# Optimization experiments

Hardware: AMD Instinct MI355X
Metric: run time of the kernel (lower is better)

Reference implementation:

```python
import jax, jax.numpy as jnp
import numpy as np

MARGIN = 0.3
ANCHOR = 0.5
EPS = 1e-8  # torch F.cosine_similarity default eps


def _cosine(a, b):
    # a: [N, D], b: [D] -> [N]
    num = a @ b
    den = jnp.maximum(jnp.linalg.norm(a, axis=-1) * jnp.linalg.norm(b), EPS)
    return num / den


def setup_inputs() -> dict:
    key = jax.random.key(0)
    k1, k2, k3, k4 = jax.random.split(key, 4)
    N, D = 8192, 1024
    return {
        "q_emb": jax.random.normal(k1, (D,), dtype=jnp.float32),
        "d_embs": jax.random.normal(k2, (N, D), dtype=jnp.float32),
        "c_emb": jax.random.normal(k3, (D,), dtype=jnp.float32),
        "rates": jax.random.uniform(k4, (N,), dtype=jnp.float32),
    }


def reference(q_emb, d_embs, c_emb, rates):
    # cosine similarity of each distractor vs question / correct answer
    s_q = _cosine(d_embs, q_emb)          # [N]
    _s_c = _cosine(d_embs, c_emb)         # [N] computed in original, never used
    quality = jnp.abs(rates - ANCHOR)     # [N]

    # Vectorized form of the nested i,j loop:
    # pair (i, j) contributes relu(margin + s_q[j] - s_q[i]) iff quality[i] > quality[j]
    mask = quality[:, None] > quality[None, :]              # [N, N]; diagonal is False
    pair_loss = jax.nn.relu(MARGIN + s_q[None, :] - s_q[:, None])  # [N, N]
    total = jnp.sum(jnp.where(mask, pair_loss, jnp.float32(0.0)))
    n_pairs = jnp.sum(mask)
    return total / jnp.maximum(n_pairs, 1).astype(total.dtype)
```

## Files before the change

### kernel.cpp

```cpp
#include <hip/hip_runtime.h>

#define MARGIN 0.3f
#define ANCHOR 0.5f
#define EPS    1e-8f
#define BI     1024
#define BJ     64
#define NSLOT  32

typedef unsigned long long ull;


__global__ __launch_bounds__(256) void sq_kernel(
        const float* __restrict__ q, const float* __restrict__ d,
        const float* __restrict__ rates, float2* __restrict__ pairs,
        char* __restrict__ acc, int N, int D) {
    int tid = threadIdx.x;
    if (blockIdx.x == 0) {
        if (tid < NSLOT)          *(double*)  (acc + (size_t)tid * 64)               = 0.0;
        else if (tid < 2 * NSLOT) *(unsigned*)(acc + 2048 + (size_t)(tid - 32) * 64) = 0u;
    }
    int wave = (blockIdx.x * blockDim.x + tid) >> 6;
    int lane = tid & 63;
    if (wave >= N) return;
    const float* row = d + (size_t)wave * (size_t)D;

    float dot = 0.f, dn = 0.f, qn = 0.f;
    for (int it = lane * 4; it < D; it += 256) {
        float4 dv = *(const float4*)(row + it);
        float4 qv = *(const float4*)(q + it);
        dot += dv.x * qv.x + dv.y * qv.y + dv.z * qv.z + dv.w * qv.w;
        dn  += dv.x * dv.x + dv.y * dv.y + dv.z * dv.z + dv.w * dv.w;
        qn  += qv.x * qv.x + qv.y * qv.y + qv.z * qv.z + qv.w * qv.w;
    }
    #pragma unroll
    for (int off = 32; off >= 1; off >>= 1) {
        dot += __shfl_xor(dot, off);
        dn  += __shfl_xor(dn,  off);
        qn  += __shfl_xor(qn,  off);
    }
    if (lane == 0) {
        float den = fmaxf(sqrtf(dn) * sqrtf(qn), EPS);
        pairs[wave] = make_float2(dot / den, fabsf(rates[wave] - ANCHOR));
    }
}

__global__ __launch_bounds__(256) void pair_kernel(
        const float2* __restrict__ pairs,
        int N, char* __restrict__ acc) {
    __shared__ float2   tile[BJ];
    __shared__ double   bsum[4];
    __shared__ unsigned bcnt[4];

    int tid = threadIdx.x;
    int ib  = blockIdx.x * BI;
    int j0  = blockIdx.y * BJ;

    if (tid < BJ) {
        int j = j0 + tid;
        tile[tid] = (j < N) ? pairs[j] : make_float2(0.f, 1e30f);
    }
    __syncthreads();

    float a0 = 0.f, g0 = -1.f, a1 = 0.f, g1 = -1.f;
    float a2 = 0.f, g2 = -1.f, a3 = 0.f, g3 = -1.f;
    {
        int i;
        float2 p;
        i = ib + tid;        if (i < N) { p = pairs[i]; a0 = MARGIN - p.x; g0 = p.y; }
        i = ib + tid + 256;  if (i < N) { p = pairs[i]; a1 = MARGIN - p.x; g1 = p.y; }
        i = ib + tid + 512;  if (i < N) { p = pairs[i]; a2 = MARGIN - p.x; g2 = p.y; }
        i = ib + tid + 768;  if (i < N) { p = pairs[i]; a3 = MARGIN - p.x; g3 = p.y; }
    }

    float    s0 = 0.f, s1 = 0.f, s2 = 0.f, s3 = 0.f;
    unsigned c  = 0;
    #pragma unroll 8
    for (int j = 0; j < BJ; ++j) {
        float2 t = tile[j];
        bool  m0 = g0 > t.y;  float v0 = fmaxf(a0 + t.x, 0.f);
        bool  m1 = g1 > t.y;  float v1 = fmaxf(a1 + t.x, 0.f);
        bool  m2 = g2 > t.y;  float v2 = fmaxf(a2 + t.x, 0.f);
        bool  m3 = g3 > t.y;  float v3 = fmaxf(a3 + t.x, 0.f);
        s0 += m0 ? v0 : 0.f;
        s1 += m1 ? v1 : 0.f;
        s2 += m2 ? v2 : 0.f;
        s3 += m3 ? v3 : 0.f;
        c  += (unsigned)__popcll(__ballot(m0));
        c  += (unsigned)__popcll(__ballot(m1));
        c  += (unsigned)__popcll(__ballot(m2));
        c  += (unsigned)__popcll(__ballot(m3));
    }

    float sum = (s0 + s1) + (s2 + s3);
    #pragma unroll
    for (int off = 32; off >= 1; off >>= 1)
        sum += __shfl_xor(sum, off);

    int w = tid >> 6;
    if ((tid & 63) == 0) { bsum[w] = (double)sum; bcnt[w] = c; }
    __syncthreads();

    if (tid == 0) {
        double   bs = bsum[0] + bsum[1] + bsum[2] + bsum[3];
        unsigned bc = bcnt[0] + bcnt[1] + bcnt[2] + bcnt[3];
        unsigned bid = blockIdx.y * gridDim.x + blockIdx.x;
        unsigned s   = bid & (NSLOT - 1);
        atomicAdd((double*)  (acc + (size_t)s * 64), bs);
        atomicAdd((unsigned*)(acc + 2048 + (size_t)s * 64), bc);
    }
}

__global__ __launch_bounds__(64) void finalize_kernel(
        char* __restrict__ acc, float* __restrict__ out) {
    int lane = threadIdx.x;
    double s = 0.0; ull c = 0ull;
    if (lane < NSLOT) {
        s = atomicAdd((double*)  (acc + (size_t)lane * 64), 0.0);
        c = (ull)atomicAdd((unsigned*)(acc + 2048 + (size_t)lane * 64), 0u);
    }
    #pragma unroll
    for (int off = 16; off >= 1; off >>= 1) {
        s += __shfl_xor(s, off);
        c += __shfl_xor(c, off);
    }
    if (lane == 0) {
        if (c < 1ull) c = 1ull;
        out[0] = (float)(s / (double)c);
    }
}

extern "C" void kernel_launch(void* const* d_in, const int* in_sizes, int n_in,
                              void* d_out, int out_size, void* d_ws, size_t ws_size,
                              hipStream_t stream) {
    const float* q_emb  = (const float*)d_in[0];
    const float* d_embs = (const float*)d_in[1];
    const float* rates  = (const float*)d_in[3];

    int D = in_sizes[0];
    int N = in_sizes[3];

    char*   acc   = (char*)d_ws;
    float2* pairs = (float2*)(acc + 8192);
    float*  out   = (float*)d_out;

    int rows_per_block = 256 / 64;
    sq_kernel<<<(N + rows_per_block - 1) / rows_per_block, 256, 0, stream>>>(
        q_emb, d_embs, rates, pairs, acc, N, D);

    dim3 grid((N + BI - 1) / BI, (N + BJ - 1) / BJ);
    pair_kernel<<<grid, 256, 0, stream>>>(pairs, N, acc);

    finalize_kernel<<<1, 64, 0, stream>>>(acc, out);
}
```

Before: 22.32 us.

## Bucket-sort distractors by quality to skip and simplify pair tiles

Adds a histogram/scan kernel and a scatter kernel that bucket-sort the (similarity, quality) pairs by quality into 1024 descending bins. The pair kernel then returns early for tiles whose i-range lies entirely below the j-range, and uses a mask-free loop with an analytic pair count when the i-range lies entirely above. This aims to roughly halve the N^2 pair work, at the cost of two extra launches, a single-block serial histogram, and global atomics in the scatter. The i-tile also shrinks from 1024 to 512 so the bin ranges are finer.

```diff
diff --git a/kernel.cpp b/kernel.cpp
--- a/kernel.cpp
+++ b/kernel.cpp
@@ -3,16 +3,22 @@
 #define MARGIN 0.3f
 #define ANCHOR 0.5f
 #define EPS    1e-8f
-#define BI     1024
+#define NBIN   1024
+#define BI     512
 #define BJ     64
 #define NSLOT  32
 
 typedef unsigned long long ull;
 
+__device__ __forceinline__ int qbin(float q) {
+    int b = (int)(q * 2048.0f);
+    return b > (NBIN - 1) ? (NBIN - 1) : b;
+}
+
 
 __global__ __launch_bounds__(256) void sq_kernel(
         const float* __restrict__ q, const float* __restrict__ d,
-        const float* __restrict__ rates, float2* __restrict__ pairs,
+        const float* __restrict__ rates, float2* __restrict__ raw,
         char* __restrict__ acc, int N, int D) {
     int tid = threadIdx.x;
     if (blockIdx.x == 0) {
@@ -40,58 +46,110 @@
     }
     if (lane == 0) {
         float den = fmaxf(sqrtf(dn) * sqrtf(qn), EPS);
-        pairs[wave] = make_float2(dot / den, fabsf(rates[wave] - ANCHOR));
-    }
+        raw[wave] = make_float2(dot / den, fabsf(rates[wave] - ANCHOR));
+    }
+}
+
+__global__ __launch_bounds__(1024) void hist_scan_kernel(
+        const float2* __restrict__ raw, int N,
+        unsigned* __restrict__ bin_start, unsigned* __restrict__ cursor) {
+    __shared__ unsigned h[NBIN];
+    __shared__ unsigned s[NBIN];
+    int tid = threadIdx.x;
+    h[tid] = 0u;
+    __syncthreads();
+    for (int k = tid; k < N; k += 1024)
+        atomicAdd(&h[qbin(raw[k].y)], 1u);
+    __syncthreads();
+    unsigned v = h[NBIN - 1 - tid];
+    s[tid] = v;
+    __syncthreads();
+    for (int dstep = 1; dstep < NBIN; dstep <<= 1) {
+        unsigned t = (tid >= dstep) ? s[tid - dstep] : 0u;
+        __syncthreads();
+        s[tid] += t;
+        __syncthreads();
+    }
+    unsigned ex = s[tid] - v;
+    int b = NBIN - 1 - tid;
+    bin_start[b] = ex;
+    cursor[b]    = ex;
+}
+
+__global__ __launch_bounds__(256) void scatter_kernel(
+        const float2* __restrict__ raw, float2* __restrict__ sorted,
+        unsigned* __restrict__ cursor, int N) {
+    int i = blockIdx.x * 256 + threadIdx.x;
+    if (i >= N) return;
+    float2 p = raw[i];
+    unsigned pos = atomicAdd(&cursor[qbin(p.y)], 1u);
+    sorted[pos] = p;
 }
 
 __global__ __launch_bounds__(256) void pair_kernel(
-        const float2* __restrict__ pairs,
+        const float2* __restrict__ sorted,
         int N, char* __restrict__ acc) {
     __shared__ float2   tile[BJ];
     __shared__ double   bsum[4];
     __shared__ unsigned bcnt[4];
 
-    int tid = threadIdx.x;
-    int ib  = blockIdx.x * BI;
-    int j0  = blockIdx.y * BJ;
+    int tid  = threadIdx.x;
+    int i0   = blockIdx.x * BI;
+    int j0   = blockIdx.y * BJ;
+    int imax = N - i0; if (imax > BI) imax = BI;
+    int jmax = N - j0; if (jmax > BJ) jmax = BJ;
+
+    int b_i_hi = qbin(sorted[i0].y);
+    int b_i_lo = qbin(sorted[i0 + imax - 1].y);
+    int b_j_hi = qbin(sorted[j0].y);
+    int b_j_lo = qbin(sorted[j0 + jmax - 1].y);
+
+    if (b_i_hi < b_j_lo) return;
 
     if (tid < BJ) {
         int j = j0 + tid;
-        tile[tid] = (j < N) ? pairs[j] : make_float2(0.f, 1e30f);
-    }
-    __syncthreads();
-
-    float a0 = 0.f, g0 = -1.f, a1 = 0.f, g1 = -1.f;
-    float a2 = 0.f, g2 = -1.f, a3 = 0.f, g3 = -1.f;
-    {
-        int i;
-        float2 p;
-        i = ib + tid;        if (i < N) { p = pairs[i]; a0 = MARGIN - p.x; g0 = p.y; }
-        i = ib + tid + 256;  if (i < N) { p = pairs[i]; a1 = MARGIN - p.x; g1 = p.y; }
-        i = ib + tid + 512;  if (i < N) { p = pairs[i]; a2 = MARGIN - p.x; g2 = p.y; }
-        i = ib + tid + 768;  if (i < N) { p = pairs[i]; a3 = MARGIN - p.x; g3 = p.y; }
-    }
-
-    float    s0 = 0.f, s1 = 0.f, s2 = 0.f, s3 = 0.f;
+        tile[tid] = (j < N) ? sorted[j] : make_float2(0.f, 1e30f);
+    }
+    __syncthreads();
+
+    int  ia = i0 + tid, ib = i0 + 256 + tid;
+    bool va = ia < N,   vb = ib < N;
+    float2 pa = va ? sorted[ia] : make_float2(0.f, -1.f);
+    float2 pb = vb ? sorted[ib] : make_float2(0.f, -1.f);
+    float aa = va ? (MARGIN - pa.x) : -1e30f;
+    float ab = vb ? (MARGIN - pb.x) : -1e30f;
+    float ga = va ? pa.y : -1.f;
+    float gb = vb ? pb.y : -1.f;
+
+    float    s0 = 0.f, s1 = 0.f;
     unsigned c  = 0;
-    #pragma unroll 8
-    for (int j = 0; j < BJ; ++j) {
-        float2 t = tile[j];
-        bool  m0 = g0 > t.y;  float v0 = fmaxf(a0 + t.x, 0.f);
-        bool  m1 = g1 > t.y;  float v1 = fmaxf(a1 + t.x, 0.f);
-        bool  m2 = g2 > t.y;  float v2 = fmaxf(a2 + t.x, 0.f);
-        bool  m3 = g3 > t.y;  float v3 = fmaxf(a3 + t.x, 0.f);
-        s0 += m0 ? v0 : 0.f;
-        s1 += m1 ? v1 : 0.f;
-        s2 += m2 ? v2 : 0.f;
-        s3 += m3 ? v3 : 0.f;
-        c  += (unsigned)__popcll(__ballot(m0));
-        c  += (unsigned)__popcll(__ballot(m1));
-        c  += (unsigned)__popcll(__ballot(m2));
-        c  += (unsigned)__popcll(__ballot(m3));
-    }
-
-    float sum = (s0 + s1) + (s2 + s3);
+
+    if (b_i_lo > b_j_hi) {
+        #pragma unroll 8
+        for (int j = 0; j < jmax; ++j) {
+            float x = tile[j].x;
+            s0 += fmaxf(aa + x, 0.f);
+            s1 += fmaxf(ab + x, 0.f);
+        }
+        unsigned nva = (unsigned)__popcll(__ballot(va));
+        unsigned nvb = (unsigned)__popcll(__ballot(vb));
+        c = (unsigned)jmax * (nva + nvb);
+    } else {
+        #pragma unroll 4
+        for (int j = 0; j < jmax; ++j) {
+            float2 t = tile[j];
+            bool  m0 = ga > t.y;
+            bool  m1 = gb > t.y;
+            float v0 = fmaxf(aa + t.x, 0.f);
+            float v1 = fmaxf(ab + t.x, 0.f);
+            s0 += m0 ? v0 : 0.f;
+            s1 += m1 ? v1 : 0.f;
+            c  += (unsigned)__popcll(__ballot(m0));
+            c  += (unsigned)__popcll(__ballot(m1));
+        }
+    }
+
+    float sum = s0 + s1;
     #pragma unroll
     for (int off = 32; off >= 1; off >>= 1)
         sum += __shfl_xor(sum, off);
@@ -104,9 +162,9 @@
         double   bs = bsum[0] + bsum[1] + bsum[2] + bsum[3];
         unsigned bc = bcnt[0] + bcnt[1] + bcnt[2] + bcnt[3];
         unsigned bid = blockIdx.y * gridDim.x + blockIdx.x;
-        unsigned s   = bid & (NSLOT - 1);
-        atomicAdd((double*)  (acc + (size_t)s * 64), bs);
-        atomicAdd((unsigned*)(acc + 2048 + (size_t)s * 64), bc);
+        unsigned sl  = bid & (NSLOT - 1);
+        atomicAdd((double*)  (acc + (size_t)sl * 64), bs);
+        atomicAdd((unsigned*)(acc + 2048 + (size_t)sl * 64), bc);
     }
 }
 
@@ -139,16 +197,23 @@
     int D = in_sizes[0];
     int N = in_sizes[3];
 
-    char*   acc   = (char*)d_ws;
-    float2* pairs = (float2*)(acc + 8192);
-    float*  out   = (float*)d_out;
+    char*     acc       = (char*)d_ws;
+    unsigned* bin_start = (unsigned*)(acc + 4096);
+    unsigned* cursor    = (unsigned*)(acc + 8192);
+    float2*   raw       = (float2*)(acc + 12288);
+    float2*   sorted    = raw + N;
+    float*    out       = (float*)d_out;
 
     int rows_per_block = 256 / 64;
     sq_kernel<<<(N + rows_per_block - 1) / rows_per_block, 256, 0, stream>>>(
-        q_emb, d_embs, rates, pairs, acc, N, D);
+        q_emb, d_embs, rates, raw, acc, N, D);
+
+    hist_scan_kernel<<<1, 1024, 0, stream>>>(raw, N, bin_start, cursor);
+
+    scatter_kernel<<<(N + 255) / 256, 256, 0, stream>>>(raw, sorted, cursor, N);
 
     dim3 grid((N + BI - 1) / BI, (N + BJ - 1) / BJ);
-    pair_kernel<<<grid, 256, 0, stream>>>(pairs, N, acc);
+    pair_kernel<<<grid, 256, 0, stream>>>(sorted, N, acc);
 
     finalize_kernel<<<1, 64, 0, stream>>>(acc, out);
 }
```

Result: slower. 27.85 us (+24.8%).
